# Kernel tuning notes

Measured on AMD Instinct MI355X. Metric: run time of the kernel, lower is better.

The kernel has to match this reference:

```python
import jax, jax.numpy as jnp
import numpy as np

N = 100000   # num visited nodes
D = 128      # emb_dim
B = 1024     # num queries (eg_idx groups)
DEG = 256    # edges per query group (fixed, > K so topk always prunes)
E = B * DEG  # 262144 edges
K = 20       # max_attended_edges
RATIO = 0.0  # ratio_update
NEG_SLOPE = 0.01  # LeakyReLU default


def segment_softmax(logits, seg, num_segments):
    m = jax.ops.segment_max(logits, seg, num_segments=num_segments)
    ex = jnp.exp(logits - m[seg])
    s = jax.ops.segment_sum(ex, seg, num_segments=num_segments)
    return ex / s[seg]


def setup_inputs() -> dict:
    key = jax.random.key(0)
    ks = jax.random.split(key, 11)
    node_score = jax.random.uniform(ks[0], (N,), dtype=jnp.float32)
    node_repr = jax.random.normal(ks[1], (N, D), dtype=jnp.float32)
    rel_emb = jax.random.normal(ks[2], (E, D), dtype=jnp.float32)
    q_src_emb = jax.random.normal(ks[3], (B, D), dtype=jnp.float32)
    q_rel_emb = jax.random.normal(ks[4], (B, D), dtype=jnp.float32)
    # G3: Linear(4D, 4D, bias=False), init normal std sqrt(2/dim_in)
    Wq = jax.random.normal(ks[5], (4 * D, 4 * D), dtype=jnp.float32) * np.sqrt(2.0 / (4 * D))
    Wk = jax.random.normal(ks[6], (4 * D, 4 * D), dtype=jnp.float32) * np.sqrt(2.0 / (4 * D))
    # linear_between_steps: Linear(D, D) xavier
    W_lin = jax.random.normal(ks[7], (D, D), dtype=jnp.float32) * np.sqrt(2.0 / (2 * D))
    b_lin = jnp.zeros((D,), dtype=jnp.float32)
    # edges: [E, 8]; col0 = eg_idx (sorted, fixed DEG per group), col6 = vi, col7 = vj
    eg = jnp.repeat(jnp.arange(B, dtype=jnp.int32), DEG)
    vi = jax.random.randint(ks[8], (E,), 0, N, dtype=jnp.int32)
    vj = jax.random.randint(ks[9], (E,), 0, N, dtype=jnp.int32)
    z = jnp.zeros((E,), dtype=jnp.int32)
    edges = jnp.stack([eg, z, z, z, z, z, vi, vj], axis=1)
    return {
        "node_score": node_score, "node_repr": node_repr, "rel_emb": rel_emb,
        "q_src_emb": q_src_emb, "q_rel_emb": q_rel_emb,
        "Wq": Wq, "Wk": Wk, "W_lin": W_lin, "b_lin": b_lin, "edges": edges,
    }


def reference(node_score, node_repr, rel_emb, q_src_emb, q_rel_emb, Wq, Wk, W_lin, b_lin, edges):
    eg = edges[:, 0]
    vi = edges[:, 6]
    vj = edges[:, 7]
    # --- G3 attention score over edges ---
    hvi = node_repr[vi]           # [E, D]
    hvj = node_repr[vj]           # [E, D]
    qst = q_src_emb[eg]           # [E, D]
    qr = q_rel_emb[eg]            # [E, D]
    left = jnp.concatenate([hvi, rel_emb, qst, qr], axis=-1)   # [E, 4D]
    right = jnp.concatenate([hvj, rel_emb, qst, qr], axis=-1)  # [E, 4D]
    logits = jnp.sum((left @ Wq.T) * (right @ Wk.T), axis=-1)  # [E]
    # --- segment softmax over source node vi ---
    sm = segment_softmax(logits, vi, N)
    src_score = node_score[vi]
    target_score = sm * src_score
    # --- per-query-group top-k edge pruning (fixed DEG per group) ---
    topk_vals, topk_idx = jax.lax.top_k(target_score.reshape(B, DEG), K)  # [B, K]
    flat_idx = (topk_idx + jnp.arange(B, dtype=topk_idx.dtype)[:, None] * DEG).reshape(-1)  # [B*K]
    p_vi = vi[flat_idx]
    p_vj = vj[flat_idx]
    p_sm = sm[flat_idx]
    p_src = src_score[flat_idx]
    # --- node score aggregation: scatter-sum sm*src_score into target node vj ---
    updated_node_score = jax.ops.segment_sum(p_sm * p_src, p_vj, num_segments=N)
    # --- node representation update (sparse transition + identity fill) ---
    agg = jax.ops.segment_sum((1.0 - RATIO) * p_sm[:, None] * node_repr[p_vj], p_vi, num_segments=N)
    appears = jnp.zeros((N,), dtype=jnp.float32).at[p_vi].set(1.0)
    self_coef = jnp.where(appears > 0, RATIO, 1.0)[:, None]
    updated_repr = agg + self_coef * node_repr
    # --- bypass_forward: LeakyReLU(Linear) ---
    updated_repr = jax.nn.leaky_relu(updated_repr @ W_lin.T + b_lin, NEG_SLOPE)
    return updated_node_score, updated_repr
```

## Files before the change

### kernel.cpp

```cpp
#include <hip/hip_runtime.h>

#define NN 100000
#define BQ 1024
#define EE 262144
#define KTOP 20

typedef unsigned long long ull;
typedef __attribute__((ext_vector_type(8))) short bf16x8;
typedef __attribute__((ext_vector_type(4))) float f32x4;

__device__ __forceinline__ ull enc64(double d) {
  ull u = (ull)__double_as_longlong(d);
  return (u >> 63) ? ~u : (u | 0x8000000000000000ull);
}
__device__ __forceinline__ double dec64(ull u) {
  ull b = (u >> 63) ? (u & 0x7FFFFFFFFFFFFFFFull) : ~u;
  return __longlong_as_double((long long)b);
}

__device__ __forceinline__ unsigned short f2bf(float f) {
  unsigned u = __float_as_uint(f);
  u += 0x7fff + ((u >> 16) & 1);
  return (unsigned short)(u >> 16);
}
__device__ __forceinline__ float bf2f(unsigned short h) {
  return __uint_as_float(((unsigned)h) << 16);
}
__device__ __forceinline__ void cvt8(float4 x, float4 y, bf16x8& hi, bf16x8& lo) {
  float a[8] = {x.x, x.y, x.z, x.w, y.x, y.y, y.z, y.w};
#pragma unroll
  for (int j = 0; j < 8; j++) {
    unsigned short h = f2bf(a[j]);
    float r = a[j] - bf2f(h);
    hi[j] = (short)h;
    lo[j] = (short)f2bf(r);
  }
}

__global__ void k_prep(const int* __restrict__ edges, int4* __restrict__ evi,
                       int* __restrict__ vi32, ull* __restrict__ menc,
                       double* __restrict__ s, float* __restrict__ appears,
                       float* __restrict__ out_score) {
  int i = blockIdx.x * 256 + threadIdx.x;
  int st = gridDim.x * 256;
  for (int e = i; e < EE; e += st) {
    int vi = edges[(size_t)e * 8 + 6];
    evi[e] = make_int4(edges[(size_t)e * 8 + 0], vi, edges[(size_t)e * 8 + 7], 0);
    vi32[e] = vi;
  }
  for (int n = i; n < NN; n += st) {
    menc[n] = 0ull;
    s[n] = 0.0;
    appears[n] = 0.f;
    out_score[n] = 0.f;
  }
}

__global__ void k_matM(const float* __restrict__ Wq, const float* __restrict__ Wk,
                       float* __restrict__ M) {
  int x = blockIdx.x;
  int y = blockIdx.y * 256 + threadIdx.x;
  float acc = 0.f;
  for (int a = 0; a < 512; a++)
    acc += Wq[a * 512 + x] * Wk[a * 512 + y];
  M[x * 512 + y] = acc;
}

__global__ void k_transpose(const float* __restrict__ M, float* __restrict__ MT) {
  int x = blockIdx.x;
  int y = blockIdx.y * 256 + threadIdx.x;
  MT[y * 512 + x] = M[x * 512 + y];
}

__global__ void k_pack(const float* __restrict__ M, const float* __restrict__ MT,
                       const float* __restrict__ Wl,
                       short* __restrict__ wn_hi, short* __restrict__ wn_lo,
                       short* __restrict__ m11_hi, short* __restrict__ m11_lo,
                       short* __restrict__ wl_hi, short* __restrict__ wl_lo) {
  int idx = blockIdx.x * 256 + threadIdx.x;
  if (idx >= 5 * 16384) return;
  int arr = idx >> 14;
  int j16 = idx & 16383;
  int g = j16 >> 9;
  int l = (j16 >> 3) & 63;
  int jj = j16 & 7;
  int c = (g >> 2) * 16 + (l & 15);
  int k = (g & 3) * 32 + ((l >> 4) << 3) + jj;
  float v;
  short *dh, *dl;
  if (arr == 0)      { v = MT[(size_t)c * 512 + k];               dh = wn_hi;          dl = wn_lo; }
  else if (arr == 1) { v = MT[(size_t)(128 + c) * 512 + k];       dh = wn_hi + 16384;  dl = wn_lo + 16384; }
  else if (arr == 2) { v = M[(size_t)(128 + c) * 512 + k];        dh = wn_hi + 32768;  dl = wn_lo + 32768; }
  else if (arr == 3) { v = MT[(size_t)(128 + c) * 512 + 128 + k]; dh = m11_hi;         dl = m11_lo; }
  else               { v = Wl[(size_t)c * 128 + k];               dh = wl_hi;          dl = wl_lo; }
  unsigned short h = f2bf(v);
  float r = v - bf2f(h);
  dh[j16] = (short)h;
  dl[j16] = (short)f2bf(r);
}

__global__ void k_pq(const float* __restrict__ M, const float* __restrict__ MT,
                     const float* __restrict__ qsA, const float* __restrict__ qrA,
                     float* __restrict__ Qv, double* __restrict__ cq) {
  int b = blockIdx.x, d = threadIdx.x;
  __shared__ float qs[128], qr[128];
  qs[d] = qsA[b * 128 + d];
  qr[d] = qrA[b * 128 + d];
  __syncthreads();
  float uh = 0, ui = 0, ur = 0;
  for (int x = 0; x < 128; x++) {
    float qsx = qs[x], qrx = qr[x];
    uh += qsx * M[(256 + x) * 512 + d]        + qrx * M[(384 + x) * 512 + d];
    ur += qsx * M[(256 + x) * 512 + 128 + d]  + qrx * M[(384 + x) * 512 + 128 + d];
    ui += qsx * MT[(256 + x) * 512 + d]       + qrx * MT[(384 + x) * 512 + d];
    ur += qsx * MT[(256 + x) * 512 + 128 + d] + qrx * MT[(384 + x) * 512 + 128 + d];
  }
  Qv[b * 384 + d]       = uh;
  Qv[b * 384 + 128 + d] = ui;
  Qv[b * 384 + 256 + d] = ur;
  float t1 = 0, t2 = 0;
  for (int y = 0; y < 128; y++) {
    float qsy = qs[y], qry = qr[y];
    t1 += qsy * MT[(256 + y) * 512 + 256 + d] + qry * MT[(384 + y) * 512 + 256 + d];
    t2 += qsy * MT[(256 + y) * 512 + 384 + d] + qry * MT[(384 + y) * 512 + 384 + d];
  }
  float cp = qs[d] * t1 + qr[d] * t2;
  for (int off = 32; off; off >>= 1) cp += __shfl_down(cp, off, 64);
  __shared__ float red[2];
  if ((d & 63) == 0) red[d >> 6] = cp;
  __syncthreads();
  if (d == 0) cq[b] = (double)(red[0] + red[1]);
}

__global__ __launch_bounds__(512) void k_gemm_node(const float* __restrict__ A,
                                                   const short* __restrict__ WT_hi,
                                                   const short* __restrict__ WT_lo,
                                                   float* __restrict__ G,
                                                   float* __restrict__ H1,
                                                   float* __restrict__ J) {
  __shared__ __align__(16) float As[64][132];
  __shared__ __align__(16) short Bh[16384];
  float* Of = (float*)Bh;
  int t = threadIdx.x;
  int row0 = blockIdx.x * 64;
  int w = t >> 6, l = t & 63;
  int rt = w & 3;
  int c0 = (w >> 2) * 4;
#pragma unroll
  for (int i = 0; i < 4; i++) {
    int fi = t + i * 512;
    int r = fi >> 5, c4 = (fi & 31) * 4;
    float4 v = make_float4(0.f, 0.f, 0.f, 0.f);
    if (row0 + r < NN) v = *(const float4*)(A + (size_t)(row0 + r) * 128 + c4);
    *(float4*)&As[r][c4] = v;
    *(bf16x8*)&Bh[fi * 8] = *(const bf16x8*)(WT_hi + fi * 8);
  }
  __syncthreads();
  int rloc = rt * 16 + (l & 15);
  int kq = (l >> 4) * 8;
  for (int panel = 0; panel < 3; panel++) {
    const short* sl = WT_lo + panel * 16384;
    bf16x8 blv[4][4];
#pragma unroll
    for (int cc = 0; cc < 4; cc++)
#pragma unroll
      for (int kt = 0; kt < 4; kt++)
        blv[cc][kt] = *(const bf16x8*)(sl + (((c0 + cc) * 4 + kt) * 64 + l) * 8);
    f32x4 acc[4];
#pragma unroll
    for (int cc = 0; cc < 4; cc++)
#pragma unroll
      for (int j = 0; j < 4; j++) acc[cc][j] = 0.f;
#pragma unroll
    for (int kt = 0; kt < 4; kt++) {
      int kb = kt * 32 + kq;
      float4 x = *(const float4*)&As[rloc][kb];
      float4 y = *(const float4*)&As[rloc][kb + 4];
      bf16x8 ah, al;
      cvt8(x, y, ah, al);
#pragma unroll
      for (int cc = 0; cc < 4; cc++) {
        int off = (((cc + c0) * 4 + kt) * 64 + l) * 8;
        bf16x8 bhv = *(const bf16x8*)&Bh[off];
        acc[cc] = __builtin_amdgcn_mfma_f32_16x16x32_bf16(ah, bhv, acc[cc], 0, 0, 0);
        acc[cc] = __builtin_amdgcn_mfma_f32_16x16x32_bf16(al, bhv, acc[cc], 0, 0, 0);
        acc[cc] = __builtin_amdgcn_mfma_f32_16x16x32_bf16(ah, blv[cc][kt], acc[cc], 0, 0, 0);
      }
    }
    __syncthreads();
#pragma unroll
    for (int cc = 0; cc < 4; cc++) {
      int col = (c0 + cc) * 16 + (l & 15);
#pragma unroll
      for (int reg = 0; reg < 4; reg++)
        Of[(rt * 16 + (l >> 4) * 4 + reg) * 128 + col] = acc[cc][reg];
    }
    __syncthreads();
    float* dst = (panel == 0) ? G : (panel == 1) ? H1 : J;
#pragma unroll
    for (int i = 0; i < 4; i++) {
      int fi = t + i * 512;
      int r = fi >> 5, c4 = (fi & 31) * 4;
      int rr = row0 + r;
      if (rr < NN) *(float4*)&dst[(size_t)rr * 128 + c4] = *(float4*)&Of[r * 128 + c4];
    }
    if (panel < 2) {
      __syncthreads();
      const short* sh = WT_hi + (panel + 1) * 16384;
#pragma unroll
      for (int i = 0; i < 4; i++) {
        int fi = t + i * 512;
        *(bf16x8*)&Bh[fi * 8] = *(const bf16x8*)(sh + fi * 8);
      }
      __syncthreads();
    }
  }
}

__global__ __launch_bounds__(512) void k_edge(const float* __restrict__ rel,
                                              const short* __restrict__ M11T_hi,
                                              const short* __restrict__ M11T_lo,
                                              const int4* __restrict__ evi,
                                              const float* __restrict__ H1,
                                              const float* __restrict__ J,
                                              const float* __restrict__ Qv,
                                              float* __restrict__ rq) {
  __shared__ __align__(16) float Rs[64][132];
  __shared__ float part[2][64];
  __shared__ float dg[64];
  int t = threadIdx.x;
  int e0 = blockIdx.x * 64;
  int w = t >> 6, l = t & 63;
  int rt = w & 3;
  int h = w >> 2;
  bf16x8 bhv[4][4], blv[4][4];
#pragma unroll
  for (int cc = 0; cc < 4; cc++)
#pragma unroll
    for (int kt = 0; kt < 4; kt++) {
      int off = (((h * 4 + cc) * 4 + kt) * 64 + l) * 8;
      bhv[cc][kt] = *(const bf16x8*)(M11T_hi + off);
      blv[cc][kt] = *(const bf16x8*)(M11T_lo + off);
    }
#pragma unroll
  for (int i = 0; i < 4; i++) {
    int fi = t + i * 512;
    int r = fi >> 5, c4 = (fi & 31) * 4;
    *(float4*)&Rs[r][c4] = *(const float4*)(rel + (size_t)(e0 + r) * 128 + c4);
  }
  __syncthreads();
  int rloc = rt * 16 + (l & 15);
  int kq = (l >> 4) * 8;
  f32x4 acc[4];
#pragma unroll
  for (int cc = 0; cc < 4; cc++)
#pragma unroll
    for (int j = 0; j < 4; j++) acc[cc][j] = 0.f;
#pragma unroll
  for (int kt = 0; kt < 4; kt++) {
    int kb = kt * 32 + kq;
    float4 x = *(const float4*)&Rs[rloc][kb];
    float4 y = *(const float4*)&Rs[rloc][kb + 4];
    bf16x8 ah, al;
    cvt8(x, y, ah, al);
#pragma unroll
    for (int cc = 0; cc < 4; cc++) {
      acc[cc] = __builtin_amdgcn_mfma_f32_16x16x32_bf16(ah, bhv[cc][kt], acc[cc], 0, 0, 0);
      acc[cc] = __builtin_amdgcn_mfma_f32_16x16x32_bf16(al, bhv[cc][kt], acc[cc], 0, 0, 0);
      acc[cc] = __builtin_amdgcn_mfma_f32_16x16x32_bf16(ah, blv[cc][kt], acc[cc], 0, 0, 0);
    }
  }
  int rq4 = (l >> 4) * 4;
  float p[4] = {0.f, 0.f, 0.f, 0.f};
#pragma unroll
  for (int cc = 0; cc < 4; cc++) {
    int c = (h * 4 + cc) * 16 + (l & 15);
#pragma unroll
    for (int reg = 0; reg < 4; reg++)
      p[reg] += acc[cc][reg] * Rs[rt * 16 + rq4 + reg][c];
  }
#pragma unroll
  for (int reg = 0; reg < 4; reg++) {
    p[reg] += __shfl_xor(p[reg], 1, 64);
    p[reg] += __shfl_xor(p[reg], 2, 64);
    p[reg] += __shfl_xor(p[reg], 4, 64);
    p[reg] += __shfl_xor(p[reg], 8, 64);
  }
  if ((l & 15) == 0) {
#pragma unroll
    for (int reg = 0; reg < 4; reg++) part[h][rt * 16 + rq4 + reg] = p[reg];
  }
  int gg = t >> 4;
  int ll = t & 15;
  int d = ll * 8;
#pragma unroll
  for (int pe = 0; pe < 2; pe++) {
    int le = gg * 2 + pe;
    int e = e0 + le;
    int4 ed = evi[e];
    const float* h1p = H1 + (size_t)ed.y * 128 + d;
    const float* jp  = J + (size_t)ed.z * 128 + d;
    const float* up  = Qv + (size_t)ed.x * 384 + 256 + d;
    float4 a0 = *(const float4*)h1p, a1 = *(const float4*)(h1p + 4);
    float4 b0 = *(const float4*)jp,  b1 = *(const float4*)(jp + 4);
    float4 u0 = *(const float4*)up,  u1 = *(const float4*)(up + 4);
    float4 r0 = *(const float4*)&Rs[le][d], r1 = *(const float4*)&Rs[le][d + 4];
    float dot = (a0.x + b0.x + u0.x) * r0.x + (a0.y + b0.y + u0.y) * r0.y
              + (a0.z + b0.z + u0.z) * r0.z + (a0.w + b0.w + u0.w) * r0.w
              + (a1.x + b1.x + u1.x) * r1.x + (a1.y + b1.y + u1.y) * r1.y
              + (a1.z + b1.z + u1.z) * r1.z + (a1.w + b1.w + u1.w) * r1.w;
    dot += __shfl_xor(dot, 1, 64);
    dot += __shfl_xor(dot, 2, 64);
    dot += __shfl_xor(dot, 4, 64);
    dot += __shfl_xor(dot, 8, 64);
    if (ll == 0) dg[le] = dot;
  }
  __syncthreads();
  if (t < 64) rq[e0 + t] = part[0][t] + part[1][t] + dg[t];
}

__global__ __launch_bounds__(256) void k_logits(const int4* __restrict__ evi,
                                                const float* __restrict__ nrep,
                                                const float* __restrict__ G,
                                                const float* __restrict__ Qv,
                                                const double* __restrict__ cq,
                                                const float* __restrict__ rq,
                                                double* __restrict__ logits,
                                                ull* __restrict__ menc) {
  int t = threadIdx.x;
  int ll = t & 15;
  int grp = (t & 63) >> 4;
  int wid = blockIdx.x * 4 + (t >> 6);
  int nw = gridDim.x * 4;
  int d = ll * 8;
  for (int e4 = wid; e4 < EE / 4; e4 += nw) {
    int e = e4 * 4 + grp;
    int4 ed = evi[e];
    int eg = ed.x, vi = ed.y, vj = ed.z;
    const float* gp = G + (size_t)vi * 128 + d;
    const float* hi = nrep + (size_t)vi * 128 + d;
    const float* hj = nrep + (size_t)vj * 128 + d;
    const float* q  = Qv + (size_t)eg * 384 + d;
    float4 g0  = *(const float4*)gp,        g1  = *(const float4*)(gp + 4);
    float4 a0  = *(const float4*)hi,        a1  = *(const float4*)(hi + 4);
    float4 b0  = *(const float4*)hj,        b1  = *(const float4*)(hj + 4);
    float4 uh0 = *(const float4*)q,         uh1 = *(const float4*)(q + 4);
    float4 ui0 = *(const float4*)(q + 128), ui1 = *(const float4*)(q + 132);
    float acc;
    acc  = (g0.x + uh0.x) * b0.x + (g0.y + uh0.y) * b0.y
         + (g0.z + uh0.z) * b0.z + (g0.w + uh0.w) * b0.w
         + (g1.x + uh1.x) * b1.x + (g1.y + uh1.y) * b1.y
         + (g1.z + uh1.z) * b1.z + (g1.w + uh1.w) * b1.w;
    acc += ui0.x * a0.x + ui0.y * a0.y + ui0.z * a0.z + ui0.w * a0.w
         + ui1.x * a1.x + ui1.y * a1.y + ui1.z * a1.z + ui1.w * a1.w;
    acc += __shfl_xor(acc, 1, 64);
    acc += __shfl_xor(acc, 2, 64);
    acc += __shfl_xor(acc, 4, 64);
    acc += __shfl_xor(acc, 8, 64);
    if (ll == 0) {
      double l2 = (double)acc + cq[eg] + (double)rq[e];
      logits[e] = l2;
      atomicMax(&menc[vi], enc64(l2));
    }
  }
}

__global__ void k_exp(const int* __restrict__ vi32, const ull* __restrict__ menc,
                      const double* __restrict__ logits, double* __restrict__ ex,
                      double* __restrict__ s) {
  int i = blockIdx.x * 256 + threadIdx.x;
  int st = gridDim.x * 256;
  for (int e = i; e < EE; e += st) {
    int vi = vi32[e];
    double m = dec64(menc[vi]);
    double v = exp(logits[e] - m);
    ex[e] = v;
    atomicAdd(&s[vi], v);
  }
}

__global__ void k_zero_agg(float4* __restrict__ agg) {
  int i = blockIdx.x * 256 + threadIdx.x;
  int st = gridDim.x * 256;
  const int n4 = NN * 32;
  for (int n = i; n < n4; n += st) agg[n] = make_float4(0.f, 0.f, 0.f, 0.f);
}

__global__ void k_topk(const double* __restrict__ ex, const double* __restrict__ s,
                       const float* __restrict__ nscore, const int4* __restrict__ evi,
                       const float* __restrict__ nrep, float* __restrict__ out_score,
                       float* __restrict__ agg, float* __restrict__ appears) {
  int b = blockIdx.x, t = threadIdx.x;
  int e = b * 256 + t;
  int vi_t = evi[e].y;
  double v = ex[e] / s[vi_t] * (double)nscore[vi_t];
  __shared__ double cv[80];
  __shared__ int ci[80];
  __shared__ int winners[KTOP];
  int w = t >> 6;
  for (int k = 0; k < KTOP; k++) {
    double bv = v;
    int bi = t;
    for (int off = 32; off; off >>= 1) {
      double ov = __shfl_down(bv, off, 64);
      int oi = __shfl_down(bi, off, 64);
      if (ov > bv || (ov == bv && oi < bi)) { bv = ov; bi = oi; }
    }
    bi = __shfl(bi, 0, 64);
    if ((t & 63) == 0) { cv[w * KTOP + k] = bv; ci[w * KTOP + k] = bi; }
    if (t == bi) v = -1.0;
  }
  __syncthreads();
  if (t < 64) {
    double v0 = cv[t];
    int i0 = ci[t];
    double v1 = (t < 16) ? cv[64 + t] : -2.0;
    int i1 = (t < 16) ? ci[64 + t] : (1 << 30);
    for (int k = 0; k < KTOP; k++) {
      double bv; int bi;
      if (v1 > v0 || (v1 == v0 && i1 < i0)) { bv = v1; bi = i1; }
      else                                  { bv = v0; bi = i0; }
      for (int off = 32; off; off >>= 1) {
        double ov = __shfl_down(bv, off, 64);
        int oi = __shfl_down(bi, off, 64);
        if (ov > bv || (ov == bv && oi < bi)) { bv = ov; bi = oi; }
      }
      bi = __shfl(bi, 0, 64);
      if (t == 0) winners[k] = bi;
      if (i0 == bi) v0 = -2.0;
      if (i1 == bi) v1 = -2.0;
    }
  }
  __syncthreads();
  for (int k = 0; k < KTOP; k++) {
    int we = b * 256 + winners[k];
    int4 ew = evi[we];
    int vi = ew.y, vj = ew.z;
    double sm = ex[we] / s[vi];
    if (t < 128) {
      atomicAdd(&agg[(size_t)vi * 128 + t], (float)sm * nrep[(size_t)vj * 128 + t]);
    } else if (t == 128) {
      atomicAdd(&out_score[vj], (float)(sm * (double)nscore[vi]));
    } else if (t == 129) {
      appears[vi] = 1.f;
    }
  }
}

__global__ __launch_bounds__(512) void k_final(const float* __restrict__ agg,
                                               const float* __restrict__ appears,
                                               const float* __restrict__ nrep,
                                               const short* __restrict__ Wl_hi,
                                               const short* __restrict__ Wl_lo,
                                               const float* __restrict__ bl,
                                               float* __restrict__ outr) {
  __shared__ __align__(16) float Xs[64][132];
  __shared__ __align__(16) short Bh[16384];
  int t = threadIdx.x;
  int row0 = blockIdx.x * 64;
  int w = t >> 6, l = t & 63;
  int rt = w & 3;
  int c0 = (w >> 2) * 4;
  bf16x8 blv[4][4];
#pragma unroll
  for (int cc = 0; cc < 4; cc++)
#pragma unroll
    for (int kt = 0; kt < 4; kt++)
      blv[cc][kt] = *(const bf16x8*)(Wl_lo + (((c0 + cc) * 4 + kt) * 64 + l) * 8);
#pragma unroll
  for (int i = 0; i < 4; i++) {
    int fi = t + i * 512;
    int r = fi >> 5, c4 = (fi & 31) * 4;
    int rr = row0 + r;
    float4 v = make_float4(0.f, 0.f, 0.f, 0.f);
    if (rr < NN) {
      float4 ag = *(const float4*)(agg + (size_t)rr * 128 + c4);
      float4 h = *(const float4*)(nrep + (size_t)rr * 128 + c4);
      float coef = (appears[rr] > 0.f) ? 0.f : 1.f;
      v.x = ag.x + coef * h.x;
      v.y = ag.y + coef * h.y;
      v.z = ag.z + coef * h.z;
      v.w = ag.w + coef * h.w;
    }
    *(float4*)&Xs[r][c4] = v;
    *(bf16x8*)&Bh[fi * 8] = *(const bf16x8*)(Wl_hi + fi * 8);
  }
  __syncthreads();
  int rloc = rt * 16 + (l & 15);
  int kq = (l >> 4) * 8;
  f32x4 acc[4];
#pragma unroll
  for (int cc = 0; cc < 4; cc++)
#pragma unroll
    for (int j = 0; j < 4; j++) acc[cc][j] = 0.f;
#pragma unroll
  for (int kt = 0; kt < 4; kt++) {
    int kb = kt * 32 + kq;
    float4 x = *(const float4*)&Xs[rloc][kb];
    float4 y = *(const float4*)&Xs[rloc][kb + 4];
    bf16x8 ah, al;
    cvt8(x, y, ah, al);
#pragma unroll
    for (int cc = 0; cc < 4; cc++) {
      int off = (((c0 + cc) * 4 + kt) * 64 + l) * 8;
      bf16x8 bhv = *(const bf16x8*)&Bh[off];
      acc[cc] = __builtin_amdgcn_mfma_f32_16x16x32_bf16(ah, bhv, acc[cc], 0, 0, 0);
      acc[cc] = __builtin_amdgcn_mfma_f32_16x16x32_bf16(al, bhv, acc[cc], 0, 0, 0);
      acc[cc] = __builtin_amdgcn_mfma_f32_16x16x32_bf16(ah, blv[cc][kt], acc[cc], 0, 0, 0);
    }
  }
  __syncthreads();
#pragma unroll
  for (int cc = 0; cc < 4; cc++) {
    int col = (c0 + cc) * 16 + (l & 15);
#pragma unroll
    for (int reg = 0; reg < 4; reg++)
      Xs[rt * 16 + (l >> 4) * 4 + reg][col] = acc[cc][reg];
  }
  __syncthreads();
#pragma unroll
  for (int i = 0; i < 4; i++) {
    int fi = t + i * 512;
    int r = fi >> 5, c4 = (fi & 31) * 4;
    int rr = row0 + r;
    if (rr < NN) {
      float4 v = *(float4*)&Xs[r][c4];
      float4 bb = *(const float4*)&bl[c4];
      float4 o;
      o.x = v.x + bb.x; o.x = (o.x > 0.f) ? o.x : 0.01f * o.x;
      o.y = v.y + bb.y; o.y = (o.y > 0.f) ? o.y : 0.01f * o.y;
      o.z = v.z + bb.z; o.z = (o.z > 0.f) ? o.z : 0.01f * o.z;
      o.w = v.w + bb.w; o.w = (o.w > 0.f) ? o.w : 0.01f * o.w;
      *(float4*)&outr[(size_t)rr * 128 + c4] = o;
    }
  }
}

extern "C" void kernel_launch(void* const* d_in, const int* in_sizes, int n_in,
                              void* d_out, int out_size, void* d_ws, size_t ws_size,
                              hipStream_t stream) {
  const float* node_score = (const float*)d_in[0];
  const float* node_repr  = (const float*)d_in[1];
  const float* rel_emb    = (const float*)d_in[2];
  const float* q_src      = (const float*)d_in[3];
  const float* q_rel      = (const float*)d_in[4];
  const float* Wq         = (const float*)d_in[5];
  const float* Wk         = (const float*)d_in[6];
  const float* W_lin      = (const float*)d_in[7];
  const float* b_lin      = (const float*)d_in[8];
  const int*   edges      = (const int*)d_in[9];

  char* ws = (char*)d_ws;
  size_t off = 0;
  auto carve = [&](size_t bytes) -> void* {
    void* p = ws + off;
    off += (bytes + 255) & ~(size_t)255;
    return p;
  };
  float*  M      = (float*)carve(512 * 512 * 4);
  float*  MT     = (float*)carve(512 * 512 * 4);
  short*  wn_hi  = (short*)carve(3 * 16384 * 2);
  short*  wn_lo  = (short*)carve(3 * 16384 * 2);
  short*  m11_hi = (short*)carve(16384 * 2);
  short*  m11_lo = (short*)carve(16384 * 2);
  short*  wl_hi  = (short*)carve(16384 * 2);
  short*  wl_lo  = (short*)carve(16384 * 2);
  float*  Qv     = (float*)carve((size_t)BQ * 384 * 4);
  double* cq     = (double*)carve((size_t)BQ * 8);
  double* logits = (double*)carve((size_t)EE * 8);
  float*  rq     = (float*)carve((size_t)EE * 4);
  ull*    menc   = (ull*)carve((size_t)NN * 8);
  double* s      = (double*)carve((size_t)NN * 8);
  double* ex     = (double*)carve((size_t)EE * 8);
  float*  appears= (float*)carve((size_t)NN * 4);
  int4*   evi    = (int4*)carve((size_t)EE * 16);
  int*    vi32   = (int*)carve((size_t)EE * 4);
  float*  G      = (float*)carve((size_t)NN * 128 * 4);
  float*  H1     = (float*)carve((size_t)NN * 128 * 4);
  float*  J      = (float*)carve((size_t)NN * 128 * 4);
  float*  agg    = G;

  float* out_score = (float*)d_out;
  float* out_repr  = (float*)d_out + NN;

  k_prep<<<1024, 256, 0, stream>>>(edges, evi, vi32, menc, s, appears, out_score);
  k_matM<<<dim3(512, 2), 256, 0, stream>>>(Wq, Wk, M);
  k_transpose<<<dim3(512, 2), 256, 0, stream>>>(M, MT);
  k_pack<<<320, 256, 0, stream>>>(M, MT, W_lin, wn_hi, wn_lo, m11_hi, m11_lo, wl_hi, wl_lo);
  k_pq<<<BQ, 128, 0, stream>>>(M, MT, q_src, q_rel, Qv, cq);
  k_gemm_node<<<1563, 512, 0, stream>>>(node_repr, wn_hi, wn_lo, G, H1, J);
  k_edge<<<4096, 512, 0, stream>>>(rel_emb, m11_hi, m11_lo, evi, H1, J, Qv, rq);
  k_logits<<<8192, 256, 0, stream>>>(evi, node_repr, G, Qv, cq, rq, logits, menc);
  k_zero_agg<<<2048, 256, 0, stream>>>((float4*)agg);
  k_exp<<<1024, 256, 0, stream>>>(vi32, menc, logits, ex, s);
  k_topk<<<BQ, 256, 0, stream>>>(ex, s, node_score, evi, node_repr, out_score, agg, appears);
  k_final<<<1563, 512, 0, stream>>>(agg, appears, node_repr, wl_hi, wl_lo, b_lin, out_repr);
}
```

Baseline: 427.8 us.

## Fuse small kernels and stage edge-kernel weights and query vector in LDS

The transpose is folded into the M product kernel, and the agg zeroing is folded into the exp kernel, which now launches twice as many blocks. In k_edge the hi half of the M11 weights moves from registers into shared memory (32KB), and each block loads its per-group query slice once into shared memory instead of gathering it per edge. This cuts launch overhead, register pressure and redundant global loads. The costs are higher LDS use per block, launch_bounds(512,1) capping occupancy, and extra LDS reads inside the MFMA loop.

```diff
diff --git a/kernel.cpp b/kernel.cpp
--- a/kernel.cpp
+++ b/kernel.cpp
@@ -57,19 +57,14 @@
 }
 
 __global__ void k_matM(const float* __restrict__ Wq, const float* __restrict__ Wk,
-                       float* __restrict__ M) {
+                       float* __restrict__ M, float* __restrict__ MT) {
   int x = blockIdx.x;
   int y = blockIdx.y * 256 + threadIdx.x;
   float acc = 0.f;
   for (int a = 0; a < 512; a++)
     acc += Wq[a * 512 + x] * Wk[a * 512 + y];
   M[x * 512 + y] = acc;
-}
-
-__global__ void k_transpose(const float* __restrict__ M, float* __restrict__ MT) {
-  int x = blockIdx.x;
-  int y = blockIdx.y * 256 + threadIdx.x;
-  MT[y * 512 + x] = M[x * 512 + y];
+  MT[y * 512 + x] = acc;
 }
 
 __global__ void k_pack(const float* __restrict__ M, const float* __restrict__ MT,
@@ -217,40 +212,42 @@
   }
 }
 
-__global__ __launch_bounds__(512) void k_edge(const float* __restrict__ rel,
-                                              const short* __restrict__ M11T_hi,
-                                              const short* __restrict__ M11T_lo,
-                                              const int4* __restrict__ evi,
-                                              const float* __restrict__ H1,
-                                              const float* __restrict__ J,
-                                              const float* __restrict__ Qv,
-                                              float* __restrict__ rq) {
+__global__ __launch_bounds__(512, 1) void k_edge(const float* __restrict__ rel,
+                                                 const short* __restrict__ M11T_hi,
+                                                 const short* __restrict__ M11T_lo,
+                                                 const int4* __restrict__ evi,
+                                                 const float* __restrict__ H1,
+                                                 const float* __restrict__ J,
+                                                 const float* __restrict__ Qv,
+                                                 float* __restrict__ rq) {
   __shared__ __align__(16) float Rs[64][132];
+  __shared__ __align__(16) short Bh[16384];
   __shared__ float part[2][64];
   __shared__ float dg[64];
+  __shared__ float urs[128];
   int t = threadIdx.x;
   int e0 = blockIdx.x * 64;
+  int eg = e0 >> 8;
   int w = t >> 6, l = t & 63;
   int rt = w & 3;
   int h = w >> 2;
-  bf16x8 bhv[4][4], blv[4][4];
+  bf16x8 blv[4][4];
 #pragma unroll
   for (int cc = 0; cc < 4; cc++)
 #pragma unroll
-    for (int kt = 0; kt < 4; kt++) {
-      int off = (((h * 4 + cc) * 4 + kt) * 64 + l) * 8;
-      bhv[cc][kt] = *(const bf16x8*)(M11T_hi + off);
-      blv[cc][kt] = *(const bf16x8*)(M11T_lo + off);
-    }
+    for (int kt = 0; kt < 4; kt++)
+      blv[cc][kt] = *(const bf16x8*)(M11T_lo + (((h * 4 + cc) * 4 + kt) * 64 + l) * 8);
 #pragma unroll
   for (int i = 0; i < 4; i++) {
     int fi = t + i * 512;
     int r = fi >> 5, c4 = (fi & 31) * 4;
     *(float4*)&Rs[r][c4] = *(const float4*)(rel + (size_t)(e0 + r) * 128 + c4);
-  }
-  __syncthreads();
+    *(bf16x8*)&Bh[fi * 8] = *(const bf16x8*)(M11T_hi + fi * 8);
+  }
+  if (t < 128) urs[t] = Qv[(size_t)eg * 384 + 256 + t];
+  __syncthreads();
+  int kq = (l >> 4) * 8;
   int rloc = rt * 16 + (l & 15);
-  int kq = (l >> 4) * 8;
   f32x4 acc[4];
 #pragma unroll
   for (int cc = 0; cc < 4; cc++)
@@ -265,8 +262,9 @@
     cvt8(x, y, ah, al);
 #pragma unroll
     for (int cc = 0; cc < 4; cc++) {
-      acc[cc] = __builtin_amdgcn_mfma_f32_16x16x32_bf16(ah, bhv[cc][kt], acc[cc], 0, 0, 0);
-      acc[cc] = __builtin_amdgcn_mfma_f32_16x16x32_bf16(al, bhv[cc][kt], acc[cc], 0, 0, 0);
+      bf16x8 bhv = *(const bf16x8*)&Bh[(((h * 4 + cc) * 4 + kt) * 64 + l) * 8];
+      acc[cc] = __builtin_amdgcn_mfma_f32_16x16x32_bf16(ah, bhv, acc[cc], 0, 0, 0);
+      acc[cc] = __builtin_amdgcn_mfma_f32_16x16x32_bf16(al, bhv, acc[cc], 0, 0, 0);
       acc[cc] = __builtin_amdgcn_mfma_f32_16x16x32_bf16(ah, blv[cc][kt], acc[cc], 0, 0, 0);
     }
   }
@@ -293,6 +291,7 @@
   int gg = t >> 4;
   int ll = t & 15;
   int d = ll * 8;
+  float4 u0 = *(const float4*)&urs[d], u1 = *(const float4*)&urs[d + 4];
 #pragma unroll
   for (int pe = 0; pe < 2; pe++) {
     int le = gg * 2 + pe;
@@ -300,10 +299,8 @@
     int4 ed = evi[e];
     const float* h1p = H1 + (size_t)ed.y * 128 + d;
     const float* jp  = J + (size_t)ed.z * 128 + d;
-    const float* up  = Qv + (size_t)ed.x * 384 + 256 + d;
     float4 a0 = *(const float4*)h1p, a1 = *(const float4*)(h1p + 4);
     float4 b0 = *(const float4*)jp,  b1 = *(const float4*)(jp + 4);
-    float4 u0 = *(const float4*)up,  u1 = *(const float4*)(up + 4);
     float4 r0 = *(const float4*)&Rs[le][d], r1 = *(const float4*)&Rs[le][d + 4];
     float dot = (a0.x + b0.x + u0.x) * r0.x + (a0.y + b0.y + u0.y) * r0.y
               + (a0.z + b0.z + u0.z) * r0.z + (a0.w + b0.w + u0.w) * r0.w
@@ -316,7 +313,7 @@
     if (ll == 0) dg[le] = dot;
   }
   __syncthreads();
-  if (t < 64) rq[e0 + t] = part[0][t] + part[1][t] + dg[t];
+  if (t < 64) rq[e0 + t] = (part[0][t] + part[1][t]) + dg[t];
 }
 
 __global__ __launch_bounds__(256) void k_logits(const int4* __restrict__ evi,
@@ -367,7 +364,7 @@
 
 __global__ void k_exp(const int* __restrict__ vi32, const ull* __restrict__ menc,
                       const double* __restrict__ logits, double* __restrict__ ex,
-                      double* __restrict__ s) {
+                      double* __restrict__ s, float4* __restrict__ agg) {
   int i = blockIdx.x * 256 + threadIdx.x;
   int st = gridDim.x * 256;
   for (int e = i; e < EE; e += st) {
@@ -377,11 +374,6 @@
     ex[e] = v;
     atomicAdd(&s[vi], v);
   }
-}
-
-__global__ void k_zero_agg(float4* __restrict__ agg) {
-  int i = blockIdx.x * 256 + threadIdx.x;
-  int st = gridDim.x * 256;
   const int n4 = NN * 32;
   for (int n = i; n < n4; n += st) agg[n] = make_float4(0.f, 0.f, 0.f, 0.f);
 }
@@ -584,15 +576,13 @@
   float* out_repr  = (float*)d_out + NN;
 
   k_prep<<<1024, 256, 0, stream>>>(edges, evi, vi32, menc, s, appears, out_score);
-  k_matM<<<dim3(512, 2), 256, 0, stream>>>(Wq, Wk, M);
-  k_transpose<<<dim3(512, 2), 256, 0, stream>>>(M, MT);
+  k_matM<<<dim3(512, 2), 256, 0, stream>>>(Wq, Wk, M, MT);
   k_pack<<<320, 256, 0, stream>>>(M, MT, W_lin, wn_hi, wn_lo, m11_hi, m11_lo, wl_hi, wl_lo);
   k_pq<<<BQ, 128, 0, stream>>>(M, MT, q_src, q_rel, Qv, cq);
   k_gemm_node<<<1563, 512, 0, stream>>>(node_repr, wn_hi, wn_lo, G, H1, J);
   k_edge<<<4096, 512, 0, stream>>>(rel_emb, m11_hi, m11_lo, evi, H1, J, Qv, rq);
   k_logits<<<8192, 256, 0, stream>>>(evi, node_repr, G, Qv, cq, rq, logits, menc);
-  k_zero_agg<<<2048, 256, 0, stream>>>((float4*)agg);
-  k_exp<<<1024, 256, 0, stream>>>(vi32, menc, logits, ex, s);
+  k_exp<<<2048, 256, 0, stream>>>(vi32, menc, logits, ex, s, (float4*)agg);
   k_topk<<<BQ, 256, 0, stream>>>(ex, s, node_score, evi, node_repr, out_score, agg, appears);
   k_final<<<1563, 512, 0, stream>>>(agg, appears, node_repr, wl_hi, wl_lo, b_lin, out_repr);
 }
```

Result: faster. 388.0 us (-9.3%).
